# Optimization experiments

Measured on AMD Instinct MI355X. Metric: run time of the kernel, lower is better.

## Reference

```python
import jax, jax.numpy as jnp
import numpy as np

E = 8192
K = 16
P = E * K
HIDDEN = 128
HEADS = 8
HEAD_DIM = HIDDEN // HEADS  # 16
NRAD = 64
CUTOFF = 10.0
EPS = 1e-5


def _rbf(d):
    # Gaussian radial basis expansion on [0, cutoff]
    centers = jnp.linspace(0.0, CUTOFF, NRAD)
    width = CUTOFF / NRAD
    return jnp.exp(-(((d[..., None] - centers) / width) ** 2))  # [..., NRAD]


def setup_inputs() -> dict:
    key = jax.random.key(0)
    ks = jax.random.split(key, 24)

    def lin_w(k, fi, fo):
        s = 1.0 / np.sqrt(fi)
        return jax.random.uniform(k, (fi, fo), minval=-s, maxval=s, dtype=jnp.float32)

    def lin_b(k, fi, fo):
        s = 1.0 / np.sqrt(fi)
        return jax.random.uniform(k, (fo,), minval=-s, maxval=s, dtype=jnp.float32)

    edge_features = jax.random.normal(ks[0], (E, HIDDEN), dtype=jnp.float32)
    edge_coords = jax.random.normal(ks[1], (E, 3), dtype=jnp.float32) * 3.0
    # K neighbors per edge: row index repeated, neighbor index random
    src = jnp.repeat(jnp.arange(E, dtype=jnp.int32), K)
    dst = jax.random.randint(ks[2], (P,), 0, E, dtype=jnp.int32)
    edge_pairs = jnp.stack([src, dst], axis=-1)  # [P, 2]

    mlp_in = HEAD_DIM * 2 + NRAD + 1  # 97
    return {
        "edge_features": edge_features,
        "edge_coords": edge_coords,
        "Wq": lin_w(ks[3], HIDDEN, HIDDEN),
        "Wk": lin_w(ks[4], HIDDEN, HIDDEN),
        "Wv": lin_w(ks[5], HIDDEN, HIDDEN),
        "W1": lin_w(ks[6], mlp_in, HIDDEN), "b1": lin_b(ks[7], mlp_in, HIDDEN),
        "W2": lin_w(ks[8], HIDDEN, HIDDEN), "b2": lin_b(ks[9], HIDDEN, HIDDEN),
        "W3": lin_w(ks[10], HIDDEN, HEADS), "b3": lin_b(ks[11], HIDDEN, HEADS),
        "Wg1": lin_w(ks[12], HEAD_DIM, HIDDEN), "bg1": lin_b(ks[13], HEAD_DIM, HIDDEN),
        "Wg2": lin_w(ks[14], HIDDEN, 1), "bg2": lin_b(ks[15], HIDDEN, 1),
        "Wo": lin_w(ks[16], HIDDEN, HIDDEN), "bo": lin_b(ks[17], HIDDEN, HIDDEN),
        "gamma": jnp.ones((HIDDEN,), jnp.float32),
        "beta": jnp.zeros((HIDDEN,), jnp.float32),
        "edge_pairs": edge_pairs,
    }


def reference(edge_features, edge_coords, Wq, Wk, Wv, W1, b1, W2, b2, W3, b3,
              Wg1, bg1, Wg2, bg2, Wo, bo, gamma, beta, edge_pairs):
    E_ = edge_features.shape[0]
    src = edge_pairs[:, 0]
    dst = edge_pairs[:, 1]
    silu = jax.nn.silu

    q = (edge_features @ Wq).reshape(E_, HEADS, HEAD_DIM)
    k = (edge_features @ Wk).reshape(E_, HEADS, HEAD_DIM)
    v = (edge_features @ Wv).reshape(E_, HEADS, HEAD_DIM)

    coord_diff = edge_coords[src] - edge_coords[dst]        # [P, 3]
    dist = jnp.sqrt(jnp.sum(coord_diff * coord_diff, -1))   # [P]
    rb = _rbf(dist)                                         # [P, NRAD]

    feats = []
    coords = edge_coords
    for h in range(HEADS):  # fixed small loop over structurally distinct heads
        qp = q[src, h]                                      # [P, HEAD_DIM]
        kp = k[dst, h]
        vp = v[dst, h]
        dot = jnp.sum(qp * kp, -1, keepdims=True)           # [P, 1]
        x = jnp.concatenate([qp, kp, rb, dot], axis=-1)     # [P, 97]
        hmid = silu(silu(x @ W1 + b1) @ W2 + b2)            # [P, HIDDEN]
        scores = (hmid @ W3 + b3)[:, h]                     # [P]
        # scatter softmax over destination rows (src index)
        m = jax.ops.segment_max(scores, src, num_segments=E_)
        w = jnp.exp(scores - m[src])
        denom = jax.ops.segment_sum(w, src, num_segments=E_)
        attn = w / denom[src]                               # [P]
        agg = jax.ops.segment_sum(attn[:, None] * vp, src, num_segments=E_)
        feats.append(agg)
        # equivariant coordinate update
        gate = jax.nn.sigmoid(silu(vp @ Wg1 + bg1) @ Wg2 + bg2)  # [P, 1]
        cu = jax.ops.segment_sum(attn[:, None] * gate * coord_diff, src,
                                 num_segments=E_)
        coords = coords + cu / HEADS

    uf = jnp.concatenate(feats, axis=-1)                    # [E, HIDDEN]
    y = edge_features + uf @ Wo + bo
    mean = jnp.mean(y, -1, keepdims=True)
    var = jnp.mean((y - mean) ** 2, -1, keepdims=True)
    yn = (y - mean) / jnp.sqrt(var + EPS) * gamma + beta
    return yn, coords
```

## Files before the change

kernel.cpp:

```cpp
#include <hip/hip_runtime.h>
#include <hip/hip_bf16.h>
#include <math.h>

#define E_N   8192
#define K_N   16
#define HID   128
#define HEADS 8
#define HD    16
#define NRAD  64

typedef unsigned short ushort_t;
typedef __attribute__((ext_vector_type(8))) short bf16x8;
typedef __attribute__((ext_vector_type(4))) float f32x4;
typedef __attribute__((ext_vector_type(2))) float f32x2;

__device__ __forceinline__ float fast_rcp(float x){ return __builtin_amdgcn_rcpf(x); }
__device__ __forceinline__ float silu_f(float x){ return x * fast_rcp(1.f + __expf(-x)); }
__device__ __forceinline__ float sigmoid_f(float x){ return fast_rcp(1.f + __expf(-x)); }

__device__ __forceinline__ ushort_t f2b(float x){
  union { __hip_bfloat16 b; ushort_t u; } cv;
  cv.b = __float2bfloat16(x);
  return cv.u;
}
__device__ __forceinline__ unsigned int pk_bf16(float a, float b){
  unsigned int r;
  asm volatile("v_cvt_pk_bf16_f32 %0, %1, %2" : "=v"(r) : "v"(a), "v"(b));
  return r;
}

__device__ __forceinline__ unsigned int silu2(f32x2 x){
  f32x2 t;
  t.x = __expf(-x.x);
  t.y = __expf(-x.y);
  f32x2 d = t + 1.f;
  f32x2 r;
  r.x = fast_rcp(d.x);
  r.y = fast_rcp(d.y);
  f32x2 y = x * r;
  return pk_bf16(y.x, y.y);
}

__device__ __forceinline__ void* lds_h(ushort_t* base, int row, int col){
  unsigned int byte = ((unsigned int)(row*256 + col*2)) ^ (((unsigned int)(row & 7)) << 4);
  return (void*)(reinterpret_cast<char*>(base) + byte);
}

__global__ __launch_bounds__(256) void qkv_kernel(
    const float* __restrict__ ef,
    const float* __restrict__ Wq, const float* __restrict__ Wk, const float* __restrict__ Wv,
    float* __restrict__ q, float* __restrict__ k, float* __restrict__ v)
{
  __shared__ float efl[16][128];
  const int t = threadIdx.x;
  const int base = blockIdx.x * 16;
  for (int idx = t; idx < 16*128; idx += 256)
    efl[idx>>7][idx&127] = ef[base*128 + idx];
  __syncthreads();

  const int j = t & 127, half = t >> 7;
  float aq[8], ak[8], av[8];
  #pragma unroll
  for (int r=0;r<8;r++){ aq[r]=0.f; ak[r]=0.f; av[r]=0.f; }
  for (int i=0;i<128;i++){
    float wq = Wq[i*128+j], wk = Wk[i*128+j], wv = Wv[i*128+j];
    #pragma unroll
    for (int r=0;r<8;r++){
      float x = efl[half*8+r][i];
      aq[r] += x*wq; ak[r] += x*wk; av[r] += x*wv;
    }
  }
  #pragma unroll
  for (int r=0;r<8;r++){
    int row = base + half*8 + r;
    q[row*128+j]=aq[r]; k[row*128+j]=ak[r]; v[row*128+j]=av[r];
  }
}

__global__ __launch_bounds__(256) void gate_kernel(
    const float* __restrict__ v,
    const float* __restrict__ Wg1, const float* __restrict__ bg1,
    const float* __restrict__ Wg2, const float* __restrict__ bg2,
    float* __restrict__ gate)
{
  const int e = blockIdx.x;
  const int t = threadIdx.x;
  const int h = t >> 5, l = t & 31;
  float vp[16];
  #pragma unroll
  for (int i=0;i<16;i++) vp[i] = v[e*128 + h*16 + i];
  float part = 0.f;
  #pragma unroll
  for (int jj=0;jj<4;jj++){
    int j = l + jj*32;
    float a = bg1[j];
    #pragma unroll
    for (int i=0;i<16;i++) a += vp[i]*Wg1[i*128+j];
    part += silu_f(a) * Wg2[j];
  }
  #pragma unroll
  for (int off=16; off>=1; off>>=1) part += __shfl_xor(part, off, 64);
  if (l==0) gate[e*8+h] = sigmoid_f(part + bg2[0]);
}

__global__ __launch_bounds__(256) void wprep_kernel(
    const float* __restrict__ W1, const float* __restrict__ W2, const float* __restrict__ W3,
    const float* __restrict__ b1,
    ushort_t* __restrict__ W1f, ushort_t* __restrict__ W2f, ushort_t* __restrict__ W3f)
{
  int idx = blockIdx.x*256 + threadIdx.x;
  if (idx < 32768){
    int id  = idx & 16383;
    int i  = id & 7;
    int l  = (id >> 3) & 63;
    int nf = (id >> 9) & 7;
    int ks = (id >> 12) & 3;
    int kk = ks*32 + (l>>4)*8 + i;
    int n  = (nf>>1)*32 + 2*(l&15) + (nf&1);
    if (idx < 16384){
      float val = (kk < 97) ? W1[kk*128 + n] : (kk == 97 ? b1[n] : 0.f);
      W1f[id] = f2b(val);
    } else {
      W2f[id] = f2b(W2[kk*128 + n]);
    }
  } else {
    int id = idx - 32768;
    int i  = id & 7;
    int l  = (id >> 3) & 63;
    int ks = (id >> 9) & 3;
    int kk = ks*32 + (l>>4)*8 + i;
    int n  = l & 15;
    W3f[id] = (n < 8) ? f2b(W3[kk*8 + n]) : (ushort_t)0;
  }
}

__global__ __launch_bounds__(256) void edge_attn_mfma(
    const float* __restrict__ ef, const float* __restrict__ coords,
    const float* __restrict__ q, const float* __restrict__ k, const float* __restrict__ v,
    const ushort_t* __restrict__ W1f, const ushort_t* __restrict__ W2f,
    const ushort_t* __restrict__ W3f,
    const float* __restrict__ b2, const float* __restrict__ b3,
    const float* __restrict__ Wo, const float* __restrict__ bo,
    const float* __restrict__ gamma, const float* __restrict__ beta,
    const int* __restrict__ pairs, const float* __restrict__ gate,
    float* __restrict__ out_y, float* __restrict__ out_c)
{
  __shared__ __align__(16) ushort_t BufA[128*128];
  __shared__ __align__(16) float SmallBuf[416];
  __shared__ float cd_l[16][4];
  __shared__ float gate_l[16][8];
  __shared__ int   dstl[16];

  float* sc_l   = SmallBuf;
  float* attn_l = SmallBuf + 128;
  float* feats  = SmallBuf + 256;
  float* red    = SmallBuf + 384;
  float* wopart = SmallBuf;

  const int e = blockIdx.x;
  const int t = threadIdx.x;
  const int w  = t >> 6;
  const int l  = t & 63;
  const int lr = l & 15;
  const int lg = l >> 4;

  const int pg   = lg;
  const int p    = w*4 + pg;
  const int dstp = pairs[(e*16 + p)*2 + 1];
  if (l < 4) dstl[w*4 + l] = pairs[(e*16 + w*4 + l)*2 + 1];

  float cx = coords[e*3+0]-coords[dstp*3+0];
  float cy = coords[e*3+1]-coords[dstp*3+1];
  float cz = coords[e*3+2]-coords[dstp*3+2];
  float dist = sqrtf(cx*cx+cy*cy+cz*cz);
  if (lr < 3) cd_l[p][lr] = (lr==0) ? cx : (lr==1 ? cy : cz);

  {
    int i0 = lr * 4;
    float z0 = (dist - (float)(i0+0)*(10.0f/63.0f)) * 6.4f;
    float z1 = (dist - (float)(i0+1)*(10.0f/63.0f)) * 6.4f;
    float z2 = (dist - (float)(i0+2)*(10.0f/63.0f)) * 6.4f;
    float z3 = (dist - (float)(i0+3)*(10.0f/63.0f)) * 6.4f;
    unsigned int u01 = pk_bf16(__expf(-z0*z0), __expf(-z1*z1));
    unsigned int u23 = pk_bf16(__expf(-z2*z2), __expf(-z3*z3));
    int base_row = w*32 + pg*8;
    #pragma unroll
    for (int rr=0; rr<8; rr++){
      *reinterpret_cast<unsigned int*>(lds_h(BufA, base_row+rr, 32+i0  )) = u01;
      *reinterpret_cast<unsigned int*>(lds_h(BufA, base_row+rr, 32+i0+2)) = u23;
    }
  }

  {
    const int rl  = l >> 1;
    const int hf  = l & 1;
    const int row = w*32 + rl;
    const int hh  = rl & 7;
    float dot = 0.f;
    if (hf == 0){
      const float4* qp4 = reinterpret_cast<const float4*>(q + e*128 + hh*16);
      const float4* kp4 = reinterpret_cast<const float4*>(k + dstp*128 + hh*16);
      #pragma unroll
      for (int i4=0;i4<4;i4++){
        float4 qv = qp4[i4], kv = kp4[i4];
        dot += qv.x*kv.x + qv.y*kv.y + qv.z*kv.z + qv.w*kv.w;
        *reinterpret_cast<unsigned int*>(lds_h(BufA, row, i4*4     )) = pk_bf16(qv.x, qv.y);
        *reinterpret_cast<unsigned int*>(lds_h(BufA, row, i4*4+2   )) = pk_bf16(qv.z, qv.w);
        *reinterpret_cast<unsigned int*>(lds_h(BufA, row, 16+i4*4  )) = pk_bf16(kv.x, kv.y);
        *reinterpret_cast<unsigned int*>(lds_h(BufA, row, 16+i4*4+2)) = pk_bf16(kv.z, kv.w);
      }
    }
    float dsw = __shfl_xor(dot, 1, 64);
    if (hf == 1){
      *reinterpret_cast<unsigned int*>(lds_h(BufA, row, 96)) = pk_bf16(dsw, 1.0f);
      #pragma unroll
      for (int c=98;c<128;c+=2)
        *reinterpret_cast<unsigned int*>(lds_h(BufA, row, c)) = 0u;
    }
  }
  __syncthreads();

  const int c0 = w*32 + 2*lr;
  const f32x2 b2p = { b2[c0], b2[c0+1] };

  #pragma unroll
  for (int pass=0; pass<2; ++pass){
    f32x4 acc[4][2];
    #pragma unroll
    for (int mf=0;mf<4;mf++){ acc[mf][0] = (f32x4)0.f; acc[mf][1] = (f32x4)0.f; }
    #pragma unroll
    for (int ks=0; ks<4; ks++){
      bf16x8 B0 = *reinterpret_cast<const bf16x8*>(W1f + ((ks*8 + w*2+0)*64 + l)*8);
      bf16x8 B1 = *reinterpret_cast<const bf16x8*>(W1f + ((ks*8 + w*2+1)*64 + l)*8);
      #pragma unroll
      for (int mf=0; mf<4; mf++){
        bf16x8 A = *reinterpret_cast<const bf16x8*>(lds_h(BufA, pass*64 + mf*16 + lr, ks*32 + lg*8));
        acc[mf][0] = __builtin_amdgcn_mfma_f32_16x16x32_bf16(A, B0, acc[mf][0], 0,0,0);
        acc[mf][1] = __builtin_amdgcn_mfma_f32_16x16x32_bf16(A, B1, acc[mf][1], 0,0,0);
      }
    }
    __syncthreads();
    #pragma unroll
    for (int mf=0;mf<4;mf++){
      #pragma unroll
      for (int i=0;i<4;i++){
        int row = pass*64 + mf*16 + lg*4 + i;
        f32x2 x2 = { acc[mf][0][i], acc[mf][1][i] };
        *reinterpret_cast<unsigned int*>(lds_h(BufA, row, c0)) = silu2(x2);
      }
    }
  }

  #pragma unroll
  for (int pass=0; pass<2; ++pass){
    f32x4 acc[4][2];
    #pragma unroll
    for (int mf=0;mf<4;mf++){ acc[mf][0] = (f32x4)0.f; acc[mf][1] = (f32x4)0.f; }
    #pragma unroll
    for (int ks=0; ks<4; ks++){
      bf16x8 B0 = *reinterpret_cast<const bf16x8*>(W2f + ((ks*8 + w*2+0)*64 + l)*8);
      bf16x8 B1 = *reinterpret_cast<const bf16x8*>(W2f + ((ks*8 + w*2+1)*64 + l)*8);
      #pragma unroll
      for (int mf=0; mf<4; mf++){
        bf16x8 A = *reinterpret_cast<const bf16x8*>(lds_h(BufA, pass*64 + mf*16 + lr, ks*32 + lg*8));
        acc[mf][0] = __builtin_amdgcn_mfma_f32_16x16x32_bf16(A, B0, acc[mf][0], 0,0,0);
        acc[mf][1] = __builtin_amdgcn_mfma_f32_16x16x32_bf16(A, B1, acc[mf][1], 0,0,0);
      }
    }
    __syncthreads();
    #pragma unroll
    for (int mf=0;mf<4;mf++){
      #pragma unroll
      for (int i=0;i<4;i++){
        int row = pass*64 + mf*16 + lg*4 + i;
        f32x2 x2 = (f32x2){ acc[mf][0][i], acc[mf][1][i] } + b2p;
        *reinterpret_cast<unsigned int*>(lds_h(BufA, row, c0)) = silu2(x2);
      }
    }
  }
  __syncthreads();

  {
    f32x4 a0 = (f32x4)0.f, a1 = (f32x4)0.f;
    #pragma unroll
    for (int ks=0; ks<4; ks++){
      bf16x8 B3 = *reinterpret_cast<const bf16x8*>(W3f + (ks*64 + l)*8);
      bf16x8 A0 = *reinterpret_cast<const bf16x8*>(lds_h(BufA, (w*2+0)*16 + lr, ks*32 + lg*8));
      bf16x8 A1 = *reinterpret_cast<const bf16x8*>(lds_h(BufA, (w*2+1)*16 + lr, ks*32 + lg*8));
      a0 = __builtin_amdgcn_mfma_f32_16x16x32_bf16(A0, B3, a0, 0,0,0);
      a1 = __builtin_amdgcn_mfma_f32_16x16x32_bf16(A1, B3, a1, 0,0,0);
    }
    #pragma unroll
    for (int i=0;i<4;i++){
      int rin = lg*4 + i;
      if (lr == (rin & 7)){
        sc_l[(w*2+0)*16 + rin] = a0[i] + b3[rin & 7];
        sc_l[(w*2+1)*16 + rin] = a1[i] + b3[rin & 7];
      }
    }
  }
  __syncthreads();

  if (t < 8){
    const int h = t;
    float m = -1e30f;
    for (int pp=0;pp<16;pp++) m = fmaxf(m, sc_l[pp*8+h]);
    float den = 0.f;
    for (int pp=0;pp<16;pp++){ float wgt = __expf(sc_l[pp*8+h]-m); attn_l[pp*8+h]=wgt; den += wgt; }
    float inv = fast_rcp(den);
    for (int pp=0;pp<16;pp++) attn_l[pp*8+h] *= inv;
  }
  if (t >= 128){
    int idx = t - 128; int pp = idx>>3, h = idx&7;
    gate_l[pp][h] = gate[dstl[pp]*8 + h];
  }
  __syncthreads();

  if (t < 128){
    const int h = t >> 4;
    float s = 0.f;
    #pragma unroll
    for (int pp=0;pp<16;pp++) s += attn_l[pp*8+h] * v[dstl[pp]*128 + t];
    feats[t] = s;
  }
  if (t >= 128 && t < 144){
    int pp = t-128;
    float s = 0.f;
    #pragma unroll
    for (int h=0;h<8;h++) s += attn_l[pp*8+h]*gate_l[pp][h];
    cd_l[pp][3] = s;
  }
  __syncthreads();
  if (t < 3){
    float s = 0.f;
    #pragma unroll
    for (int pp=0;pp<16;pp++) s += cd_l[pp][3]*cd_l[pp][t];
    out_c[e*3+t] = coords[e*3+t] + s*0.125f;
  }

  {
    const int col  = t & 127;
    const int half = t >> 7;
    f32x2 a2 = {0.f, 0.f};
    const float* feats2 = feats + half*64;
    const float* Wocol  = Wo + half*64*128 + col;
    #pragma unroll
    for (int iq=0; iq<32; iq++){
      f32x2 x2 = *reinterpret_cast<const f32x2*>(feats2 + iq*2);
      f32x2 w2 = { Wocol[(iq*2)*128], Wocol[(iq*2+1)*128] };
      a2 += x2 * w2;
    }
    __syncthreads();
    wopart[t] = a2.x + a2.y;
  }
  __syncthreads();

  float yv = 0.f;
  if (t < 128){
    yv = ef[e*128+t] + wopart[t] + wopart[t+128] + bo[t];
    float s1 = yv, s2 = yv*yv;
    #pragma unroll
    for (int off=32; off>=1; off>>=1){ s1 += __shfl_xor(s1,off,64); s2 += __shfl_xor(s2,off,64); }
    if ((t&63)==0){ red[(t>>6)*2+0]=s1; red[(t>>6)*2+1]=s2; }
  }
  __syncthreads();
  if (t < 128){
    float sm = red[0]+red[2], sq = red[1]+red[3];
    float mean = sm * (1.f/128.f);
    float var  = sq * (1.f/128.f) - mean*mean;
    float rstd = rsqrtf(var + 1e-5f);
    out_y[e*128+t] = (yv-mean)*rstd*gamma[t] + beta[t];
  }
}

extern "C" void kernel_launch(void* const* d_in, const int* in_sizes, int n_in,
                              void* d_out, int out_size, void* d_ws, size_t ws_size,
                              hipStream_t stream)
{
  const float* ef     = (const float*)d_in[0];
  const float* coords = (const float*)d_in[1];
  const float* Wq  = (const float*)d_in[2];
  const float* Wk  = (const float*)d_in[3];
  const float* Wv  = (const float*)d_in[4];
  const float* W1  = (const float*)d_in[5];
  const float* b1  = (const float*)d_in[6];
  const float* W2  = (const float*)d_in[7];
  const float* b2  = (const float*)d_in[8];
  const float* W3  = (const float*)d_in[9];
  const float* b3  = (const float*)d_in[10];
  const float* Wg1 = (const float*)d_in[11];
  const float* bg1 = (const float*)d_in[12];
  const float* Wg2 = (const float*)d_in[13];
  const float* bg2 = (const float*)d_in[14];
  const float* Wo  = (const float*)d_in[15];
  const float* bo  = (const float*)d_in[16];
  const float* gamma = (const float*)d_in[17];
  const float* beta  = (const float*)d_in[18];
  const int*   pairs = (const int*)d_in[19];

  float* ws   = (float*)d_ws;
  float* q    = ws;
  float* k    = q + E_N*HID;
  float* v    = k + E_N*HID;
  float* gate = v + E_N*HID;
  ushort_t* W1f = (ushort_t*)(gate + E_N*HEADS);
  ushort_t* W2f = W1f + 16384;
  ushort_t* W3f = W2f + 16384;

  qkv_kernel<<<E_N/16, 256, 0, stream>>>(ef, Wq, Wk, Wv, q, k, v);
  wprep_kernel<<<136, 256, 0, stream>>>(W1, W2, W3, b1, W1f, W2f, W3f);
  gate_kernel<<<E_N, 256, 0, stream>>>(v, Wg1, bg1, Wg2, bg2, gate);
  edge_attn_mfma<<<E_N, 256, 0, stream>>>(ef, coords, q, k, v,
      W1f, W2f, W3f, b2, b3, Wo, bo, gamma, beta, pairs, gate,
      (float*)d_out, (float*)d_out + E_N*HID);
}
```

Before: 201.7 us.

## Give each wave its own row block in the MLP to drop block barriers

Result: slower. 253.9 us (+25.8%).

```diff
diff --git a/kernel.cpp b/kernel.cpp
--- a/kernel.cpp
+++ b/kernel.cpp
@@ -218,87 +218,107 @@
         *reinterpret_cast<unsigned int*>(lds_h(BufA, row, c)) = 0u;
     }
   }
-  __syncthreads();
-
-  const int c0 = w*32 + 2*lr;
-  const f32x2 b2p = { b2[c0], b2[c0+1] };
-
-  #pragma unroll
-  for (int pass=0; pass<2; ++pass){
-    f32x4 acc[4][2];
-    #pragma unroll
-    for (int mf=0;mf<4;mf++){ acc[mf][0] = (f32x4)0.f; acc[mf][1] = (f32x4)0.f; }
+
+  f32x2 b2p[4];
+  #pragma unroll
+  for (int j=0;j<4;j++)
+    b2p[j] = *reinterpret_cast<const f32x2*>(b2 + j*32 + 2*lr);
+
+  bf16x8 Afr[2][4];
+
+  #pragma unroll
+  for (int mf2=0;mf2<2;mf2++)
+    #pragma unroll
+    for (int ks=0;ks<4;ks++)
+      Afr[mf2][ks] = *reinterpret_cast<const bf16x8*>(lds_h(BufA, w*32 + mf2*16 + lr, ks*32 + lg*8));
+
+  #pragma unroll
+  for (int npass=0; npass<2; ++npass){
+    f32x4 acc[2][4];
+    #pragma unroll
+    for (int mf2=0;mf2<2;mf2++)
+      #pragma unroll
+      for (int nf=0;nf<4;nf++) acc[mf2][nf] = (f32x4)0.f;
     #pragma unroll
     for (int ks=0; ks<4; ks++){
-      bf16x8 B0 = *reinterpret_cast<const bf16x8*>(W1f + ((ks*8 + w*2+0)*64 + l)*8);
-      bf16x8 B1 = *reinterpret_cast<const bf16x8*>(W1f + ((ks*8 + w*2+1)*64 + l)*8);
-      #pragma unroll
-      for (int mf=0; mf<4; mf++){
-        bf16x8 A = *reinterpret_cast<const bf16x8*>(lds_h(BufA, pass*64 + mf*16 + lr, ks*32 + lg*8));
-        acc[mf][0] = __builtin_amdgcn_mfma_f32_16x16x32_bf16(A, B0, acc[mf][0], 0,0,0);
-        acc[mf][1] = __builtin_amdgcn_mfma_f32_16x16x32_bf16(A, B1, acc[mf][1], 0,0,0);
-      }
-    }
-    __syncthreads();
-    #pragma unroll
-    for (int mf=0;mf<4;mf++){
+      #pragma unroll
+      for (int nf=0; nf<4; nf++){
+        bf16x8 B = *reinterpret_cast<const bf16x8*>(W1f + ((ks*8 + npass*4 + nf)*64 + l)*8);
+        acc[0][nf] = __builtin_amdgcn_mfma_f32_16x16x32_bf16(Afr[0][ks], B, acc[0][nf], 0,0,0);
+        acc[1][nf] = __builtin_amdgcn_mfma_f32_16x16x32_bf16(Afr[1][ks], B, acc[1][nf], 0,0,0);
+      }
+    }
+    #pragma unroll
+    for (int mf2=0;mf2<2;mf2++){
       #pragma unroll
       for (int i=0;i<4;i++){
-        int row = pass*64 + mf*16 + lg*4 + i;
-        f32x2 x2 = { acc[mf][0][i], acc[mf][1][i] };
-        *reinterpret_cast<unsigned int*>(lds_h(BufA, row, c0)) = silu2(x2);
-      }
-    }
-  }
-
-  #pragma unroll
-  for (int pass=0; pass<2; ++pass){
-    f32x4 acc[4][2];
-    #pragma unroll
-    for (int mf=0;mf<4;mf++){ acc[mf][0] = (f32x4)0.f; acc[mf][1] = (f32x4)0.f; }
+        int row = w*32 + mf2*16 + lg*4 + i;
+        *reinterpret_cast<unsigned int*>(lds_h(BufA, row, npass*64      + 2*lr)) =
+            silu2((f32x2){ acc[mf2][0][i], acc[mf2][1][i] });
+        *reinterpret_cast<unsigned int*>(lds_h(BufA, row, npass*64 + 32 + 2*lr)) =
+            silu2((f32x2){ acc[mf2][2][i], acc[mf2][3][i] });
+      }
+    }
+  }
+
+  #pragma unroll
+  for (int mf2=0;mf2<2;mf2++)
+    #pragma unroll
+    for (int ks=0;ks<4;ks++)
+      Afr[mf2][ks] = *reinterpret_cast<const bf16x8*>(lds_h(BufA, w*32 + mf2*16 + lr, ks*32 + lg*8));
+
+  #pragma unroll
+  for (int npass=0; npass<2; ++npass){
+    f32x4 acc[2][4];
+    #pragma unroll
+    for (int mf2=0;mf2<2;mf2++)
+      #pragma unroll
+      for (int nf=0;nf<4;nf++) acc[mf2][nf] = (f32x4)0.f;
     #pragma unroll
     for (int ks=0; ks<4; ks++){
-      bf16x8 B0 = *reinterpret_cast<const bf16x8*>(W2f + ((ks*8 + w*2+0)*64 + l)*8);
-      bf16x8 B1 = *reinterpret_cast<const bf16x8*>(W2f + ((ks*8 + w*2+1)*64 + l)*8);
-      #pragma unroll
-      for (int mf=0; mf<4; mf++){
-        bf16x8 A = *reinterpret_cast<const bf16x8*>(lds_h(BufA, pass*64 + mf*16 + lr, ks*32 + lg*8));
-        acc[mf][0] = __builtin_amdgcn_mfma_f32_16x16x32_bf16(A, B0, acc[mf][0], 0,0,0);
-        acc[mf][1] = __builtin_amdgcn_mfma_f32_16x16x32_bf16(A, B1, acc[mf][1], 0,0,0);
-      }
-    }
-    __syncthreads();
-    #pragma unroll
-    for (int mf=0;mf<4;mf++){
+      #pragma unroll
+      for (int nf=0; nf<4; nf++){
+        bf16x8 B = *reinterpret_cast<const bf16x8*>(W2f + ((ks*8 + npass*4 + nf)*64 + l)*8);
+        acc[0][nf] = __builtin_amdgcn_mfma_f32_16x16x32_bf16(Afr[0][ks], B, acc[0][nf], 0,0,0);
+        acc[1][nf] = __builtin_amdgcn_mfma_f32_16x16x32_bf16(Afr[1][ks], B, acc[1][nf], 0,0,0);
+      }
+    }
+    #pragma unroll
+    for (int mf2=0;mf2<2;mf2++){
       #pragma unroll
       for (int i=0;i<4;i++){
-        int row = pass*64 + mf*16 + lg*4 + i;
-        f32x2 x2 = (f32x2){ acc[mf][0][i], acc[mf][1][i] } + b2p;
-        *reinterpret_cast<unsigned int*>(lds_h(BufA, row, c0)) = silu2(x2);
-      }
-    }
-  }
-  __syncthreads();
+        int row = w*32 + mf2*16 + lg*4 + i;
+        *reinterpret_cast<unsigned int*>(lds_h(BufA, row, npass*64      + 2*lr)) =
+            silu2((f32x2){ acc[mf2][0][i], acc[mf2][1][i] } + b2p[npass*2+0]);
+        *reinterpret_cast<unsigned int*>(lds_h(BufA, row, npass*64 + 32 + 2*lr)) =
+            silu2((f32x2){ acc[mf2][2][i], acc[mf2][3][i] } + b2p[npass*2+1]);
+      }
+    }
+  }
 
   {
+    #pragma unroll
+    for (int mf2=0;mf2<2;mf2++)
+      #pragma unroll
+      for (int ks=0;ks<4;ks++)
+        Afr[mf2][ks] = *reinterpret_cast<const bf16x8*>(lds_h(BufA, w*32 + mf2*16 + lr, ks*32 + lg*8));
     f32x4 a0 = (f32x4)0.f, a1 = (f32x4)0.f;
     #pragma unroll
     for (int ks=0; ks<4; ks++){
       bf16x8 B3 = *reinterpret_cast<const bf16x8*>(W3f + (ks*64 + l)*8);
-      bf16x8 A0 = *reinterpret_cast<const bf16x8*>(lds_h(BufA, (w*2+0)*16 + lr, ks*32 + lg*8));
-      bf16x8 A1 = *reinterpret_cast<const bf16x8*>(lds_h(BufA, (w*2+1)*16 + lr, ks*32 + lg*8));
-      a0 = __builtin_amdgcn_mfma_f32_16x16x32_bf16(A0, B3, a0, 0,0,0);
-      a1 = __builtin_amdgcn_mfma_f32_16x16x32_bf16(A1, B3, a1, 0,0,0);
+      a0 = __builtin_amdgcn_mfma_f32_16x16x32_bf16(Afr[0][ks], B3, a0, 0,0,0);
+      a1 = __builtin_amdgcn_mfma_f32_16x16x32_bf16(Afr[1][ks], B3, a1, 0,0,0);
     }
     #pragma unroll
     for (int i=0;i<4;i++){
       int rin = lg*4 + i;
       if (lr == (rin & 7)){
-        sc_l[(w*2+0)*16 + rin] = a0[i] + b3[rin & 7];
-        sc_l[(w*2+1)*16 + rin] = a1[i] + b3[rin & 7];
-      }
-    }
-  }
+        sc_l[w*32      + rin] = a0[i] + b3[rin & 7];
+        sc_l[w*32 + 16 + rin] = a1[i] + b3[rin & 7];
+      }
+    }
+  }
+
   __syncthreads();
 
   if (t < 8){
```

## Compute QKV projections with bf16 MFMA using pre-swizzled weight fragments

Applied to the files above, without the earlier changes.

Result: faster. 195.3 us, median of 2 (-3.2%).

```diff
diff --git a/kernel.cpp b/kernel.cpp
--- a/kernel.cpp
+++ b/kernel.cpp
@@ -46,67 +46,12 @@
   return (void*)(reinterpret_cast<char*>(base) + byte);
 }
 
-__global__ __launch_bounds__(256) void qkv_kernel(
-    const float* __restrict__ ef,
-    const float* __restrict__ Wq, const float* __restrict__ Wk, const float* __restrict__ Wv,
-    float* __restrict__ q, float* __restrict__ k, float* __restrict__ v)
-{
-  __shared__ float efl[16][128];
-  const int t = threadIdx.x;
-  const int base = blockIdx.x * 16;
-  for (int idx = t; idx < 16*128; idx += 256)
-    efl[idx>>7][idx&127] = ef[base*128 + idx];
-  __syncthreads();
-
-  const int j = t & 127, half = t >> 7;
-  float aq[8], ak[8], av[8];
-  #pragma unroll
-  for (int r=0;r<8;r++){ aq[r]=0.f; ak[r]=0.f; av[r]=0.f; }
-  for (int i=0;i<128;i++){
-    float wq = Wq[i*128+j], wk = Wk[i*128+j], wv = Wv[i*128+j];
-    #pragma unroll
-    for (int r=0;r<8;r++){
-      float x = efl[half*8+r][i];
-      aq[r] += x*wq; ak[r] += x*wk; av[r] += x*wv;
-    }
-  }
-  #pragma unroll
-  for (int r=0;r<8;r++){
-    int row = base + half*8 + r;
-    q[row*128+j]=aq[r]; k[row*128+j]=ak[r]; v[row*128+j]=av[r];
-  }
-}
-
-__global__ __launch_bounds__(256) void gate_kernel(
-    const float* __restrict__ v,
-    const float* __restrict__ Wg1, const float* __restrict__ bg1,
-    const float* __restrict__ Wg2, const float* __restrict__ bg2,
-    float* __restrict__ gate)
-{
-  const int e = blockIdx.x;
-  const int t = threadIdx.x;
-  const int h = t >> 5, l = t & 31;
-  float vp[16];
-  #pragma unroll
-  for (int i=0;i<16;i++) vp[i] = v[e*128 + h*16 + i];
-  float part = 0.f;
-  #pragma unroll
-  for (int jj=0;jj<4;jj++){
-    int j = l + jj*32;
-    float a = bg1[j];
-    #pragma unroll
-    for (int i=0;i<16;i++) a += vp[i]*Wg1[i*128+j];
-    part += silu_f(a) * Wg2[j];
-  }
-  #pragma unroll
-  for (int off=16; off>=1; off>>=1) part += __shfl_xor(part, off, 64);
-  if (l==0) gate[e*8+h] = sigmoid_f(part + bg2[0]);
-}
-
 __global__ __launch_bounds__(256) void wprep_kernel(
     const float* __restrict__ W1, const float* __restrict__ W2, const float* __restrict__ W3,
     const float* __restrict__ b1,
-    ushort_t* __restrict__ W1f, ushort_t* __restrict__ W2f, ushort_t* __restrict__ W3f)
+    const float* __restrict__ Wq, const float* __restrict__ Wk, const float* __restrict__ Wv,
+    ushort_t* __restrict__ W1f, ushort_t* __restrict__ W2f, ushort_t* __restrict__ W3f,
+    ushort_t* __restrict__ Wqf, ushort_t* __restrict__ Wkf, ushort_t* __restrict__ Wvf)
 {
   int idx = blockIdx.x*256 + threadIdx.x;
   if (idx < 32768){
@@ -123,7 +68,7 @@
     } else {
       W2f[id] = f2b(W2[kk*128 + n]);
     }
-  } else {
+  } else if (idx < 34816){
     int id = idx - 32768;
     int i  = id & 7;
     int l  = (id >> 3) & 63;
@@ -131,7 +76,109 @@
     int kk = ks*32 + (l>>4)*8 + i;
     int n  = l & 15;
     W3f[id] = (n < 8) ? f2b(W3[kk*8 + n]) : (ushort_t)0;
-  }
+  } else if (idx < 83968){
+    int id = idx - 34816;
+    int m  = id >> 14;
+    int r  = id & 16383;
+    int i  = r & 7;
+    int l  = (r >> 3) & 63;
+    int nf = (r >> 9) & 7;
+    int ks = (r >> 12) & 3;
+    int kk = ks*32 + (l>>4)*8 + i;
+    int n  = nf*16 + (l&15);
+    const float* Wm = (m==0) ? Wq : ((m==1) ? Wk : Wv);
+    ushort_t*    Dm = (m==0) ? Wqf : ((m==1) ? Wkf : Wvf);
+    Dm[r] = f2b(Wm[kk*128 + n]);
+  }
+}
+
+__global__ __launch_bounds__(256) void qkv_mfma(
+    const float* __restrict__ ef,
+    const ushort_t* __restrict__ Wqf, const ushort_t* __restrict__ Wkf,
+    const ushort_t* __restrict__ Wvf,
+    float* __restrict__ q, float* __restrict__ k, float* __restrict__ v)
+{
+  __shared__ __align__(16) ushort_t EfT[64*128];
+  const int t = threadIdx.x;
+  const int w  = t >> 6;
+  const int l  = t & 63;
+  const int lr = l & 15;
+  const int lg = l >> 4;
+  const int base = blockIdx.x * 64;
+
+  {
+    int r = t >> 2, qr = t & 3;
+    const float4* src = reinterpret_cast<const float4*>(ef + (base + r)*128 + qr*32);
+    #pragma unroll
+    for (int i4=0;i4<8;i4++){
+      float4 xv = src[i4];
+      *reinterpret_cast<unsigned int*>(lds_h(EfT, r, qr*32 + i4*4    )) = pk_bf16(xv.x, xv.y);
+      *reinterpret_cast<unsigned int*>(lds_h(EfT, r, qr*32 + i4*4 + 2)) = pk_bf16(xv.z, xv.w);
+    }
+  }
+  __syncthreads();
+
+  bf16x8 Afr[4][4];
+  #pragma unroll
+  for (int mf=0;mf<4;mf++)
+    #pragma unroll
+    for (int ks=0;ks<4;ks++)
+      Afr[mf][ks] = *reinterpret_cast<const bf16x8*>(lds_h(EfT, mf*16 + lr, ks*32 + lg*8));
+
+  #pragma unroll
+  for (int m=0;m<3;m++){
+    const ushort_t* Wf = (m==0) ? Wqf : ((m==1) ? Wkf : Wvf);
+    float*          Om = (m==0) ? q   : ((m==1) ? k   : v);
+    f32x4 acc[4][2];
+    #pragma unroll
+    for (int mf=0;mf<4;mf++){ acc[mf][0] = (f32x4)0.f; acc[mf][1] = (f32x4)0.f; }
+    #pragma unroll
+    for (int ks=0; ks<4; ks++){
+      bf16x8 B0 = *reinterpret_cast<const bf16x8*>(Wf + ((ks*8 + w*2+0)*64 + l)*8);
+      bf16x8 B1 = *reinterpret_cast<const bf16x8*>(Wf + ((ks*8 + w*2+1)*64 + l)*8);
+      #pragma unroll
+      for (int mf=0; mf<4; mf++){
+        acc[mf][0] = __builtin_amdgcn_mfma_f32_16x16x32_bf16(Afr[mf][ks], B0, acc[mf][0], 0,0,0);
+        acc[mf][1] = __builtin_amdgcn_mfma_f32_16x16x32_bf16(Afr[mf][ks], B1, acc[mf][1], 0,0,0);
+      }
+    }
+    #pragma unroll
+    for (int mf=0;mf<4;mf++)
+      #pragma unroll
+      for (int nf=0;nf<2;nf++)
+        #pragma unroll
+        for (int i=0;i<4;i++){
+          int row = base + mf*16 + lg*4 + i;
+          int col = w*32 + nf*16 + lr;
+          Om[row*128 + col] = acc[mf][nf][i];
+        }
+  }
+}
+
+__global__ __launch_bounds__(256) void gate_kernel(
+    const float* __restrict__ v,
+    const float* __restrict__ Wg1, const float* __restrict__ bg1,
+    const float* __restrict__ Wg2, const float* __restrict__ bg2,
+    float* __restrict__ gate)
+{
+  const int e = blockIdx.x;
+  const int t = threadIdx.x;
+  const int h = t >> 5, l = t & 31;
+  float vp[16];
+  #pragma unroll
+  for (int i=0;i<16;i++) vp[i] = v[e*128 + h*16 + i];
+  float part = 0.f;
+  #pragma unroll
+  for (int jj=0;jj<4;jj++){
+    int j = l + jj*32;
+    float a = bg1[j];
+    #pragma unroll
+    for (int i=0;i<16;i++) a += vp[i]*Wg1[i*128+j];
+    part += silu_f(a) * Wg2[j];
+  }
+  #pragma unroll
+  for (int off=16; off>=1; off>>=1) part += __shfl_xor(part, off, 64);
+  if (l==0) gate[e*8+h] = sigmoid_f(part + bg2[0]);
 }
 
 __global__ __launch_bounds__(256) void edge_attn_mfma(
@@ -406,9 +453,13 @@
   ushort_t* W1f = (ushort_t*)(gate + E_N*HEADS);
   ushort_t* W2f = W1f + 16384;
   ushort_t* W3f = W2f + 16384;
-
-  qkv_kernel<<<E_N/16, 256, 0, stream>>>(ef, Wq, Wk, Wv, q, k, v);
-  wprep_kernel<<<136, 256, 0, stream>>>(W1, W2, W3, b1, W1f, W2f, W3f);
+  ushort_t* Wqf = W3f + 2048;
+  ushort_t* Wkf = Wqf + 16384;
+  ushort_t* Wvf = Wkf + 16384;
+
+  wprep_kernel<<<328, 256, 0, stream>>>(W1, W2, W3, b1, Wq, Wk, Wv,
+      W1f, W2f, W3f, Wqf, Wkf, Wvf);
+  qkv_mfma<<<E_N/64, 256, 0, stream>>>(ef, Wqf, Wkf, Wvf, q, k, v);
   gate_kernel<<<E_N, 256, 0, stream>>>(v, Wg1, bg1, Wg2, bg2, gate);
   edge_attn_mfma<<<E_N, 256, 0, stream>>>(ef, coords, q, k, v,
       W1f, W2f, W3f, b2, b3, Wo, bo, gamma, beta, pairs, gate,
```
